# Optimization experiments

Measured on AMD Instinct MI355X. Metric: run time of the kernel, lower is better.

The kernel has to match this reference:

```python
import jax, jax.numpy as jnp
import numpy as np

B, N, H = 16, 1024, 768
NEG_INF = -9e15
SLOPE = 0.2


def setup_inputs() -> dict:
    key = jax.random.key(0)
    k1, k2, k3, k4, k5 = jax.random.split(key, 5)
    x = jax.random.normal(k1, (B, N, H), dtype=jnp.float32)
    # node_length acts as a per-node validity mask (float, used via outer product)
    lengths = jax.random.randint(k2, (B,), N // 2, N)
    node_length = (jnp.arange(N)[None, :] < lengths[:, None]).astype(jnp.float32)
    # sparse-ish binary adjacency with self-loops
    adj = (jax.random.uniform(k3, (B, N, N)) < 0.05).astype(jnp.float32)
    adj = jnp.maximum(adj, jnp.eye(N, dtype=jnp.float32)[None])
    # params: kaiming-normal init
    W = jax.random.normal(k4, (H, H), dtype=jnp.float32) * np.sqrt(2.0 / H)
    a = jax.random.normal(k5, (2 * H, 1), dtype=jnp.float32) * np.sqrt(2.0 / (2 * H))
    return {"input": x, "node_length": node_length, "graph_structure": adj, "W": W, "a": a}


def reference(input, node_length, graph_structure, W, a):
    # node_vec = A @ X  [B,N,H]
    node_vec = jnp.matmul(graph_structure, input)
    h = jnp.matmul(node_vec, W)  # [B,N,F]
    F_ = W.shape[1]
    a1 = a[:F_, 0]   # weights on h_i
    a2 = a[F_:, 0]   # weights on h_j
    # e[b,i,j] = leaky_relu(h_i . a1 + h_j . a2)  (identical to concat+matmul with a)
    s1 = jnp.einsum("bnf,f->bn", h, a1)
    s2 = jnp.einsum("bnf,f->bn", h, a2)
    e = jax.nn.leaky_relu(s1[:, :, None] + s2[:, None, :], negative_slope=SLOPE)
    # bias = outer product of node_length; mask where adj or bias <= 1e-6
    bias = node_length[:, :, None] * node_length[:, None, :]
    valid = (graph_structure > 1e-6) & (bias > 1e-6)
    scores = jnp.where(valid, e, NEG_INF)
    attn = jax.nn.softmax(scores, axis=-1)  # attn_dropout=0 -> identity
    return node_vec, attn
```

## Files before the change

kernel.cpp:

```cpp
#include <hip/hip_runtime.h>
#include <hip/hip_bf16.h>

#define BB 16
#define NN 1024
#define HH 768
#define NEG_INF_ -9.0e15f
#define SLOPE_ 0.2f

typedef __bf16 bh8 __attribute__((ext_vector_type(8)));
typedef __bf16 bh4 __attribute__((ext_vector_type(4)));
typedef float f4 __attribute__((ext_vector_type(4)));
typedef unsigned int u32;


__device__ __forceinline__ float wave_sum0(float v) {
    #pragma unroll
    for (int off = 32; off > 0; off >>= 1) v += __shfl_down(v, off, 64);
    return v;
}
__device__ __forceinline__ float wave_sum_all(float v) {
    #pragma unroll
    for (int off = 1; off < 64; off <<= 1) v += __shfl_xor(v, off, 64);
    return v;
}
__device__ __forceinline__ float wave_max_all(float v) {
    #pragma unroll
    for (int off = 1; off < 64; off <<= 1) v = fmaxf(v, __shfl_xor(v, off, 64));
    return v;
}


__device__ __forceinline__ void gl_lds16(const void* g, void* l) {
    __builtin_amdgcn_global_load_lds(
        (const __attribute__((address_space(1))) u32*)g,
        (__attribute__((address_space(3))) u32*)l, 16, 0, 0);
}


__global__ __launch_bounds__(256) void wa_kernel(const float* __restrict__ W,
                                                 const float* __restrict__ a,
                                                 float* __restrict__ wa1,
                                                 float* __restrict__ wa2,
                                                 float* __restrict__ t1,
                                                 float* __restrict__ t2) {
    const int gid = blockIdx.x * 256 + threadIdx.x;
    if (gid < BB * NN) { t1[gid] = 0.f; t2[gid] = 0.f; }

    const int f = blockIdx.x * 4 + (threadIdx.x >> 6);
    const int lane = threadIdx.x & 63;
    const float* Wr = W + (size_t)f * HH;
    float v1 = 0.f, v2 = 0.f;
    #pragma unroll
    for (int i = 0; i < 3; i++) {
        const int h = lane * 4 + i * 256;
        const float4 w  = *(const float4*)(Wr + h);
        const float4 a1 = *(const float4*)(a + h);
        const float4 a2 = *(const float4*)(a + HH + h);
        v1 += w.x * a1.x + w.y * a1.y + w.z * a1.z + w.w * a1.w;
        v2 += w.x * a2.x + w.y * a2.y + w.z * a2.z + w.w * a2.w;
    }
    v1 = wave_sum0(v1);
    v2 = wave_sum0(v2);
    if (lane == 0) { wa1[f] = v1; wa2[f] = v2; }
}


__global__ __launch_bounds__(256) void xt_kernel(const float* __restrict__ x,
                                                 const float* __restrict__ wa1,
                                                 const float* __restrict__ wa2,
                                                 __bf16* __restrict__ xT,
                                                 float* __restrict__ t1,
                                                 float* __restrict__ t2) {
    __shared__ __bf16 T[32][36];
    const int b = blockIdx.z, nt = blockIdx.y, ht = blockIdx.x;
    const int t = threadIdx.x;
    const int r = t >> 3;
    const int c = (t & 7) * 4;
    const float4 v = *(const float4*)(x + ((size_t)b * NN + nt * 32 + r) * HH + ht * 32 + c);
    T[r][c + 0] = (__bf16)v.x; T[r][c + 1] = (__bf16)v.y;
    T[r][c + 2] = (__bf16)v.z; T[r][c + 3] = (__bf16)v.w;

    const float4 w1 = *(const float4*)(wa1 + ht * 32 + c);
    const float4 w2 = *(const float4*)(wa2 + ht * 32 + c);
    float p1 = v.x * w1.x + v.y * w1.y + v.z * w1.z + v.w * w1.w;
    float p2 = v.x * w2.x + v.y * w2.y + v.z * w2.z + v.w * w2.w;
    p1 += __shfl_down(p1, 4, 8); p1 += __shfl_down(p1, 2, 8); p1 += __shfl_down(p1, 1, 8);
    p2 += __shfl_down(p2, 4, 8); p2 += __shfl_down(p2, 2, 8); p2 += __shfl_down(p2, 1, 8);
    if ((t & 7) == 0) {
        atomicAdd(&t1[b * NN + nt * 32 + r], p1);
        atomicAdd(&t2[b * NN + nt * 32 + r], p2);
    }

    __syncthreads();
    const int h = t >> 3;
    const int nc = (t & 7) * 4;
    bh4 o = { T[nc + 0][h], T[nc + 1][h], T[nc + 2][h], T[nc + 3][h] };
    *(bh4*)(xT + ((size_t)b * HH + ht * 32 + h) * NN + nt * 32 + nc) = o;
}


__global__ __launch_bounds__(256) void s_pack_kernel(const float* __restrict__ adj,
                                                     const float* __restrict__ t1,
                                                     const float* __restrict__ t2,
                                                     float* __restrict__ s1,
                                                     float* __restrict__ s2,
                                                     __bf16* __restrict__ adjB) {
    const int row = blockIdx.x * 4 + (threadIdx.x >> 6);
    const int lane = threadIdx.x & 63;
    const int b = row >> 10;
    const float* ar = adj + (size_t)row * NN;
    __bf16* abr = adjB + (size_t)row * NN;
    const float* t1b = t1 + b * NN;
    const float* t2b = t2 + b * NN;
    float v1 = 0.f, v2 = 0.f;
    #pragma unroll
    for (int i = 0; i < 4; i++) {
        const int j = lane * 4 + i * 256;
        const float4 av = *(const float4*)(ar + j);
        const float4 u  = *(const float4*)(t1b + j);
        const float4 w  = *(const float4*)(t2b + j);
        v1 += av.x * u.x + av.y * u.y + av.z * u.z + av.w * u.w;
        v2 += av.x * w.x + av.y * w.y + av.z * w.z + av.w * w.w;
        bh4 o = { (__bf16)av.x, (__bf16)av.y, (__bf16)av.z, (__bf16)av.w };
        *(bh4*)(abr + j) = o;
    }
    v1 = wave_sum0(v1);
    v2 = wave_sum0(v2);
    if (lane == 0) { s1[row] = v1; s2[row] = v2; }
}


__global__ __launch_bounds__(256) void gemm_bf16(const __bf16* __restrict__ adjB,
                                                 const __bf16* __restrict__ xT,
                                                 float* __restrict__ out) {
    __shared__ __bf16 As[128 * 32];
    __shared__ __bf16 Bs[128 * 32];
    const int b = blockIdx.z, bm = blockIdx.y, bn = blockIdx.x;
    const int tid = threadIdx.x, lane = tid & 63, wave = tid >> 6;
    const int wr = (wave >> 1) << 6;
    const int wc = (wave & 1) << 6;
    const int quad = lane >> 4, l16 = lane & 15;

    const __bf16* Ab = adjB + ((size_t)b * NN + bm * 128) * NN;
    const __bf16* Xb = xT + ((size_t)b * HH + bn * 128) * NN;

    f4 acc[4][4];
    #pragma unroll
    for (int i = 0; i < 4; i++)
        #pragma unroll
        for (int j = 0; j < 4; j++)
            acc[i][j] = (f4){0.f, 0.f, 0.f, 0.f};

    for (int kt = 0; kt < NN; kt += 32) {
        #pragma unroll
        for (int it = 0; it < 2; it++) {
            const int c = tid + 256 * it;
            const int r = c >> 2, ko = (c & 3) * 8;
            gl_lds16(Ab + (size_t)r * NN + kt + ko, &As[r * 32 + ko]);
            gl_lds16(Xb + (size_t)r * NN + kt + ko, &Bs[r * 32 + ko]);
        }
        __syncthreads();

        bh8 af[4], bf_[4];
        #pragma unroll
        for (int i = 0; i < 4; i++)
            af[i] = *(const bh8*)&As[(wr + i * 16 + l16) * 32 + quad * 8];
        #pragma unroll
        for (int j = 0; j < 4; j++)
            bf_[j] = *(const bh8*)&Bs[(wc + j * 16 + l16) * 32 + quad * 8];

        #pragma unroll
        for (int i = 0; i < 4; i++)
            #pragma unroll
            for (int j = 0; j < 4; j++)
                acc[i][j] = __builtin_amdgcn_mfma_f32_16x16x32_bf16(af[i], bf_[j], acc[i][j], 0, 0, 0);
        __syncthreads();
    }

    float* Cb = out + (size_t)b * NN * HH + (size_t)bm * 128 * HH + bn * 128;
    const int rbase = wr + quad * 4;
    const int cbase = wc + l16;
    #pragma unroll
    for (int i = 0; i < 4; i++)
        #pragma unroll
        for (int j = 0; j < 4; j++)
            #pragma unroll
            for (int r = 0; r < 4; r++)
                Cb[(size_t)(rbase + i * 16 + r) * HH + cbase + j * 16] = acc[i][j][r];
}


__global__ __launch_bounds__(256) void softmax_kernel(const float* __restrict__ adj,
                                                      const float* __restrict__ nl,
                                                      const float* __restrict__ s1,
                                                      const float* __restrict__ s2,
                                                      float* __restrict__ attn) {
    const int row = blockIdx.x * 4 + (threadIdx.x >> 6);
    const int lane = threadIdx.x & 63;
    const int b = row >> 10, n = row & (NN - 1);
    const float* ar = adj + (size_t)row * NN;
    const float* nlb = nl + (size_t)b * NN;
    const float* s2b = s2 + (size_t)b * NN;
    const float s1v = s1[row];
    const bool rowok = nlb[n] > 1e-6f;

    f4 sc[4];
    float mx = NEG_INF_;
    #pragma unroll
    for (int i = 0; i < 4; i++) {
        const int j = lane * 4 + i * 256;
        const float4 av = *(const float4*)(ar + j);
        const float4 sv = *(const float4*)(s2b + j);
        const float4 nv = *(const float4*)(nlb + j);
        const float zs[4] = { s1v + sv.x, s1v + sv.y, s1v + sv.z, s1v + sv.w };
        const float as_[4] = { av.x, av.y, av.z, av.w };
        const float ns[4] = { nv.x, nv.y, nv.z, nv.w };
        #pragma unroll
        for (int e = 0; e < 4; e++) {
            const float z = zs[e];
            const float lr = z > 0.f ? z : SLOPE_ * z;
            const bool valid = rowok && (as_[e] > 1e-6f) && (ns[e] > 1e-6f);
            sc[i][e] = valid ? lr : NEG_INF_;
            mx = fmaxf(mx, sc[i][e]);
        }
    }
    mx = wave_max_all(mx);

    f4 ex[4];
    float sum = 0.f;
    #pragma unroll
    for (int i = 0; i < 4; i++)
        #pragma unroll
        for (int e = 0; e < 4; e++) {
            ex[i][e] = __expf(sc[i][e] - mx);
            sum += ex[i][e];
        }
    sum = wave_sum_all(sum);
    const float inv = 1.0f / sum;

    float* outr = attn + (size_t)row * NN;
    #pragma unroll
    for (int i = 0; i < 4; i++) {
        const int j = lane * 4 + i * 256;
        float4 o;
        o.x = ex[i][0] * inv; o.y = ex[i][1] * inv;
        o.z = ex[i][2] * inv; o.w = ex[i][3] * inv;
        *(float4*)(outr + j) = o;
    }
}


extern "C" void kernel_launch(void* const* d_in, const int* in_sizes, int n_in,
                              void* d_out, int out_size, void* d_ws, size_t ws_size,
                              hipStream_t stream) {
    const float* x   = (const float*)d_in[0];
    const float* nl  = (const float*)d_in[1];
    const float* adj = (const float*)d_in[2];
    const float* W   = (const float*)d_in[3];
    const float* a   = (const float*)d_in[4];

    float* out = (float*)d_out;
    float* node_vec = out;
    float* attn = out + (size_t)BB * NN * HH;

    __bf16* xT   = (__bf16*)attn;
    __bf16* adjB = (__bf16*)(attn + 6291456);

    float* ws  = (float*)d_ws;
    float* wa1 = ws;
    float* wa2 = wa1 + HH;
    float* t1  = wa2 + HH;
    float* t2  = t1 + BB * NN;
    float* s1  = t2 + BB * NN;
    float* s2  = s1 + BB * NN;

    hipLaunchKernelGGL(wa_kernel, dim3(192), dim3(256), 0, stream, W, a, wa1, wa2, t1, t2);
    hipLaunchKernelGGL(xt_kernel, dim3(24, 32, BB), dim3(256), 0, stream, x, wa1, wa2, xT, t1, t2);
    hipLaunchKernelGGL(s_pack_kernel, dim3(4096), dim3(256), 0, stream, adj, t1, t2, s1, s2, adjB);
    hipLaunchKernelGGL(gemm_bf16, dim3(6, 8, BB), dim3(256), 0, stream, adjB, xT, node_vec);
    hipLaunchKernelGGL(softmax_kernel, dim3(4096), dim3(256), 0, stream, adj, nl, s1, s2, attn);
}
```

Measured before the change: 284.4 us.

## Bit-pack adjacency mask for softmax and use swizzled 64-wide K tiles in GEMM

The pack kernel now also builds a 1-bit-per-entry adjacency mask with wave ballots. The softmax reads this mask instead of re-reading the 64MB fp32 adjacency matrix. The bf16 GEMM doubles its K tile to 64 and XOR-swizzles the LDS layout to avoid bank conflicts, which halves the barriers per K sweep. Scratch buffers move from the attn output region into the workspace, so they need a workspace of roughly 60MB.

```diff
diff --git a/kernel.cpp b/kernel.cpp
--- a/kernel.cpp
+++ b/kernel.cpp
@@ -11,6 +11,7 @@
 typedef __bf16 bh4 __attribute__((ext_vector_type(4)));
 typedef float f4 __attribute__((ext_vector_type(4)));
 typedef unsigned int u32;
+typedef unsigned long long u64;
 
 
 __device__ __forceinline__ float wave_sum0(float v) {
@@ -104,7 +105,8 @@
                                                      const float* __restrict__ t2,
                                                      float* __restrict__ s1,
                                                      float* __restrict__ s2,
-                                                     __bf16* __restrict__ adjB) {
+                                                     __bf16* __restrict__ adjB,
+                                                     u64* __restrict__ bits) {
     const int row = blockIdx.x * 4 + (threadIdx.x >> 6);
     const int lane = threadIdx.x & 63;
     const int b = row >> 10;
@@ -113,6 +115,7 @@
     const float* t1b = t1 + b * NN;
     const float* t2b = t2 + b * NN;
     float v1 = 0.f, v2 = 0.f;
+    u64 myw = 0;
     #pragma unroll
     for (int i = 0; i < 4; i++) {
         const int j = lane * 4 + i * 256;
@@ -123,18 +126,27 @@
         v2 += av.x * w.x + av.y * w.y + av.z * w.z + av.w * w.w;
         bh4 o = { (__bf16)av.x, (__bf16)av.y, (__bf16)av.z, (__bf16)av.w };
         *(bh4*)(abr + j) = o;
+        const u64 b0 = __ballot(av.x > 1e-6f);
+        const u64 b1 = __ballot(av.y > 1e-6f);
+        const u64 b2 = __ballot(av.z > 1e-6f);
+        const u64 b3 = __ballot(av.w > 1e-6f);
+        if (lane == i * 4 + 0) myw = b0;
+        if (lane == i * 4 + 1) myw = b1;
+        if (lane == i * 4 + 2) myw = b2;
+        if (lane == i * 4 + 3) myw = b3;
     }
     v1 = wave_sum0(v1);
     v2 = wave_sum0(v2);
     if (lane == 0) { s1[row] = v1; s2[row] = v2; }
+    if (lane < 16) bits[(size_t)row * 16 + lane] = myw;
 }
 
 
 __global__ __launch_bounds__(256) void gemm_bf16(const __bf16* __restrict__ adjB,
                                                  const __bf16* __restrict__ xT,
                                                  float* __restrict__ out) {
-    __shared__ __bf16 As[128 * 32];
-    __shared__ __bf16 Bs[128 * 32];
+    __shared__ __bf16 As[128 * 64];
+    __shared__ __bf16 Bs[128 * 64];
     const int b = blockIdx.z, bm = blockIdx.y, bn = blockIdx.x;
     const int tid = threadIdx.x, lane = tid & 63, wave = tid >> 6;
     const int wr = (wave >> 1) << 6;
@@ -151,29 +163,39 @@
         for (int j = 0; j < 4; j++)
             acc[i][j] = (f4){0.f, 0.f, 0.f, 0.f};
 
-    for (int kt = 0; kt < NN; kt += 32) {
-        #pragma unroll
-        for (int it = 0; it < 2; it++) {
+    for (int kt = 0; kt < NN; kt += 64) {
+        #pragma unroll
+        for (int it = 0; it < 4; it++) {
             const int c = tid + 256 * it;
-            const int r = c >> 2, ko = (c & 3) * 8;
-            gl_lds16(Ab + (size_t)r * NN + kt + ko, &As[r * 32 + ko]);
-            gl_lds16(Xb + (size_t)r * NN + kt + ko, &Bs[r * 32 + ko]);
+            const int r = c >> 3;
+            const int j = c & 7;
+            const int kc = j ^ (r & 7);
+            gl_lds16(Ab + (size_t)r * NN + kt + kc * 8, &As[r * 64 + j * 8]);
+            gl_lds16(Xb + (size_t)r * NN + kt + kc * 8, &Bs[r * 64 + j * 8]);
         }
         __syncthreads();
 
-        bh8 af[4], bf_[4];
-        #pragma unroll
-        for (int i = 0; i < 4; i++)
-            af[i] = *(const bh8*)&As[(wr + i * 16 + l16) * 32 + quad * 8];
-        #pragma unroll
-        for (int j = 0; j < 4; j++)
-            bf_[j] = *(const bh8*)&Bs[(wc + j * 16 + l16) * 32 + quad * 8];
-
-        #pragma unroll
-        for (int i = 0; i < 4; i++)
+        #pragma unroll
+        for (int s = 0; s < 2; s++) {
+            bh8 af[4], bf_[4];
             #pragma unroll
-            for (int j = 0; j < 4; j++)
-                acc[i][j] = __builtin_amdgcn_mfma_f32_16x16x32_bf16(af[i], bf_[j], acc[i][j], 0, 0, 0);
+            for (int i = 0; i < 4; i++) {
+                const int row = wr + i * 16 + l16;
+                const int jj = (s * 4 + quad) ^ (row & 7);
+                af[i] = *(const bh8*)&As[row * 64 + jj * 8];
+            }
+            #pragma unroll
+            for (int j = 0; j < 4; j++) {
+                const int row = wc + j * 16 + l16;
+                const int jj = (s * 4 + quad) ^ (row & 7);
+                bf_[j] = *(const bh8*)&Bs[row * 64 + jj * 8];
+            }
+            #pragma unroll
+            for (int i = 0; i < 4; i++)
+                #pragma unroll
+                for (int j = 0; j < 4; j++)
+                    acc[i][j] = __builtin_amdgcn_mfma_f32_16x16x32_bf16(af[i], bf_[j], acc[i][j], 0, 0, 0);
+        }
         __syncthreads();
     }
 
@@ -190,7 +212,7 @@
 }
 
 
-__global__ __launch_bounds__(256) void softmax_kernel(const float* __restrict__ adj,
+__global__ __launch_bounds__(256) void softmax_kernel(const u64* __restrict__ bits,
                                                       const float* __restrict__ nl,
                                                       const float* __restrict__ s1,
                                                       const float* __restrict__ s2,
@@ -198,7 +220,7 @@
     const int row = blockIdx.x * 4 + (threadIdx.x >> 6);
     const int lane = threadIdx.x & 63;
     const int b = row >> 10, n = row & (NN - 1);
-    const float* ar = adj + (size_t)row * NN;
+    const u64* bwr = bits + (size_t)row * 16;
     const float* nlb = nl + (size_t)b * NN;
     const float* s2b = s2 + (size_t)b * NN;
     const float s1v = s1[row];
@@ -209,17 +231,19 @@
     #pragma unroll
     for (int i = 0; i < 4; i++) {
         const int j = lane * 4 + i * 256;
-        const float4 av = *(const float4*)(ar + j);
         const float4 sv = *(const float4*)(s2b + j);
         const float4 nv = *(const float4*)(nlb + j);
+        const u64 w0 = bwr[i * 4 + 0], w1 = bwr[i * 4 + 1];
+        const u64 w2 = bwr[i * 4 + 2], w3 = bwr[i * 4 + 3];
         const float zs[4] = { s1v + sv.x, s1v + sv.y, s1v + sv.z, s1v + sv.w };
-        const float as_[4] = { av.x, av.y, av.z, av.w };
         const float ns[4] = { nv.x, nv.y, nv.z, nv.w };
+        const bool ab[4] = { (bool)((w0 >> lane) & 1ull), (bool)((w1 >> lane) & 1ull),
+                             (bool)((w2 >> lane) & 1ull), (bool)((w3 >> lane) & 1ull) };
         #pragma unroll
         for (int e = 0; e < 4; e++) {
             const float z = zs[e];
             const float lr = z > 0.f ? z : SLOPE_ * z;
-            const bool valid = rowok && (as_[e] > 1e-6f) && (ns[e] > 1e-6f);
+            const bool valid = rowok && ab[e] && (ns[e] > 1e-6f);
             sc[i][e] = valid ? lr : NEG_INF_;
             mx = fmaxf(mx, sc[i][e]);
         }
@@ -263,20 +287,20 @@
     float* node_vec = out;
     float* attn = out + (size_t)BB * NN * HH;
 
-    __bf16* xT   = (__bf16*)attn;
-    __bf16* adjB = (__bf16*)(attn + 6291456);
-
-    float* ws  = (float*)d_ws;
-    float* wa1 = ws;
+    char* wsb = (char*)d_ws;
+    float* wa1 = (float*)(wsb);
     float* wa2 = wa1 + HH;
     float* t1  = wa2 + HH;
     float* t2  = t1 + BB * NN;
     float* s1  = t2 + BB * NN;
     float* s2  = s1 + BB * NN;
+    u64*    bits = (u64*)(wsb + (1u << 20));
+    __bf16* xT   = (__bf16*)(wsb + (4u << 20));
+    __bf16* adjB = (__bf16*)(wsb + (28u << 20));
 
     hipLaunchKernelGGL(wa_kernel, dim3(192), dim3(256), 0, stream, W, a, wa1, wa2, t1, t2);
     hipLaunchKernelGGL(xt_kernel, dim3(24, 32, BB), dim3(256), 0, stream, x, wa1, wa2, xT, t1, t2);
-    hipLaunchKernelGGL(s_pack_kernel, dim3(4096), dim3(256), 0, stream, adj, t1, t2, s1, s2, adjB);
+    hipLaunchKernelGGL(s_pack_kernel, dim3(4096), dim3(256), 0, stream, adj, t1, t2, s1, s2, adjB, bits);
     hipLaunchKernelGGL(gemm_bf16, dim3(6, 8, BB), dim3(256), 0, stream, adjB, xT, node_vec);
-    hipLaunchKernelGGL(softmax_kernel, dim3(4096), dim3(256), 0, stream, adj, nl, s1, s2, attn);
-}
+    hipLaunchKernelGGL(softmax_kernel, dim3(4096), dim3(256), 0, stream, bits, nl, s1, s2, attn);
+}
```

Measured after the change: 285.5 us. About the same (+0.4%).
